# Kernel optimization log

Measured on AMD Instinct MI355X. Metric: run time of the kernel, lower is better.

The kernel has to match this reference:

```python
import jax, jax.numpy as jnp
import numpy as np

DIM = 2048
N_HEADS = 32
N_KV_HEADS = 8
HEAD_DIM = DIM // N_HEADS  # 64
N_REP = N_HEADS // N_KV_HEADS  # 4
SEQ = 2048
BSZ = 1


def _rope(x, cos, sin):
    # x: [b, s, h, hd]; cos/sin: [s, hd//2]
    x2 = x.reshape(*x.shape[:-1], HEAD_DIM // 2, 2)
    xe, xo = x2[..., 0], x2[..., 1]
    c = cos[None, :, None, :]
    s = sin[None, :, None, :]
    oe = xe * c - xo * s
    oo = xe * s + xo * c
    return jnp.stack([oe, oo], axis=-1).reshape(x.shape)


def setup_inputs() -> dict:
    key = jax.random.key(0)
    ks = jax.random.split(key, 6)
    x = jax.random.normal(ks[0], (BSZ, SEQ, DIM), dtype=jnp.float32)
    # llama-style rotary freqs
    inv = 1.0 / (10000.0 ** (np.arange(0, HEAD_DIM, 2, dtype=np.float32) / HEAD_DIM))
    t = np.arange(SEQ, dtype=np.float32)
    ang = np.outer(t, inv)  # [s, hd//2]
    freqs_cos = jnp.asarray(np.cos(ang))
    freqs_sin = jnp.asarray(np.sin(ang))
    # additive causal mask
    mask = jnp.where(jnp.tril(jnp.ones((SEQ, SEQ), bool)), 0.0, -jnp.inf).astype(jnp.float32)
    sc = 1.0 / np.sqrt(DIM)
    wq = jax.random.normal(ks[1], (DIM, N_HEADS * HEAD_DIM), jnp.float32) * sc
    wk = jax.random.normal(ks[2], (DIM, N_KV_HEADS * HEAD_DIM), jnp.float32) * sc
    wv = jax.random.normal(ks[3], (DIM, N_KV_HEADS * HEAD_DIM), jnp.float32) * sc
    wo = jax.random.normal(ks[4], (N_HEADS * HEAD_DIM, DIM), jnp.float32) * sc
    return {"x": x, "freqs_cos": freqs_cos, "freqs_sin": freqs_sin, "mask": mask,
            "wq": wq, "wk": wk, "wv": wv, "wo": wo}


def reference(x, freqs_cos, freqs_sin, mask, wq, wk, wv, wo):
    b, s, _ = x.shape
    xq = (x @ wq).reshape(b, s, N_HEADS, HEAD_DIM)
    xk = (x @ wk).reshape(b, s, N_KV_HEADS, HEAD_DIM)
    xv = (x @ wv).reshape(b, s, N_KV_HEADS, HEAD_DIM)
    xq = _rope(xq, freqs_cos, freqs_sin)
    xk = _rope(xk, freqs_cos, freqs_sin)
    # repeat_kv: expand kv heads by n_rep
    xk = jnp.repeat(xk, N_REP, axis=2)  # [b, s, H, hd]
    xv = jnp.repeat(xv, N_REP, axis=2)
    scores = jnp.einsum('bqhd,bkhd->bhqk', xq, xk) / np.sqrt(HEAD_DIM)
    scores = scores + mask[None, None, :, :]
    probs = jax.nn.softmax(scores.astype(jnp.float32), axis=-1).astype(xq.dtype)
    out = jnp.einsum('bhqk,bkhd->bqhd', probs, xv).reshape(b, s, N_HEADS * HEAD_DIM)
    return out @ wo
```

## Files before the change

kernel.cpp:

```cpp
#include <hip/hip_runtime.h>
#include <hip/hip_bf16.h>

#define SEQ  2048
#define DIM  2048
#define NQK  3072
#define NH   32
#define NKV  8
#define HD   64

typedef __attribute__((ext_vector_type(8))) short s8v;
typedef __attribute__((ext_vector_type(4))) short s4v;
typedef __attribute__((ext_vector_type(4))) float f32x4;

__device__ __forceinline__ short f2bf_bits(float f) {
    __hip_bfloat16 b = __float2bfloat16(f);
    short s; __builtin_memcpy(&s, &b, 2); return s;
}
__device__ __forceinline__ float bfbits2f(short s) {
    __hip_bfloat16 b; __builtin_memcpy(&b, &s, 2);
    return __bfloat162float(b);
}
__device__ __forceinline__ f32x4 mfma16(s8v a, s8v b, f32x4 c) {
    return __builtin_amdgcn_mfma_f32_16x16x32_bf16(a, b, c, 0, 0, 0);
}
__device__ __forceinline__ void load16_to_lds(const void* g, void* l) {
    __builtin_amdgcn_global_load_lds(
        (const __attribute__((address_space(1))) void*)g,
        (__attribute__((address_space(3))) void*)l, 16, 0, 0);
}

__global__ void cvt_f32_bf16(const float* __restrict__ src, short* __restrict__ dst) {
    int i = (blockIdx.x * 256 + threadIdx.x) * 4;
    float4 v = *(const float4*)(src + i);
    s4v o;
    o.x = f2bf_bits(v.x); o.y = f2bf_bits(v.y);
    o.z = f2bf_bits(v.z); o.w = f2bf_bits(v.w);
    *(s4v*)(dst + i) = o;
}

__global__ void transpose_cvt(const float* __restrict__ src, short* __restrict__ dst, int Cs) {
    __shared__ float tile[32][33];
    int bx = blockIdx.x * 32, by = blockIdx.y * 32;
    int tx = threadIdx.x, ty = threadIdx.y;
    #pragma unroll
    for (int j = 0; j < 32; j += 8)
        tile[ty + j][tx] = src[(size_t)(by + ty + j) * Cs + bx + tx];
    __syncthreads();
    #pragma unroll
    for (int j = 0; j < 32; j += 8)
        dst[(size_t)(bx + ty + j) * 2048 + by + tx] = f2bf_bits(tile[tx][ty + j]);
}

template<int MODE>
__global__ __launch_bounds__(256, 2)
void gemm_bt(const short* __restrict__ A, const short* __restrict__ BT,
             void* __restrict__ C, int M, int N, int K,
             short* __restrict__ vT,
             const float* __restrict__ fc, const float* __restrict__ fs)
{
    __shared__ short As[128 * 64];
    __shared__ short Bs[128 * 64];
    const int lane = threadIdx.x & 63;
    const int wid  = threadIdx.x >> 6;
    const int r = lane & 15, g = lane >> 4;
    const int bm = blockIdx.y * 128, bn = blockIdx.x * 128;
    const int wm = (wid >> 1) * 64, wn = (wid & 1) * 64;

    f32x4 acc[4][4];
    #pragma unroll
    for (int i = 0; i < 4; ++i)
        #pragma unroll
        for (int j = 0; j < 4; ++j) acc[i][j] = (f32x4){0.f, 0.f, 0.f, 0.f};

    const int srow = wid * 32 + (lane >> 3);
    const int scol = (lane & 7) * 8;

    for (int k0 = 0; k0 < K; k0 += 64) {
        #pragma unroll
        for (int s2 = 0; s2 < 4; ++s2) {
            int row = srow + s2 * 8;
            int seg = wid * 4 + s2;
            load16_to_lds(A  + (size_t)(bm + row) * K + k0 + scol, As + seg * 512);
            load16_to_lds(BT + (size_t)(bn + row) * K + k0 + scol, Bs + seg * 512);
        }
        __syncthreads();
        #pragma unroll
        for (int kk = 0; kk < 64; kk += 32) {
            s8v a[4], b[4];
            #pragma unroll
            for (int t = 0; t < 4; ++t)
                a[t] = *(const s8v*)&As[(wm + t * 16 + r) * 64 + kk + g * 8];
            #pragma unroll
            for (int t = 0; t < 4; ++t)
                b[t] = *(const s8v*)&Bs[(wn + t * 16 + r) * 64 + kk + g * 8];
            __builtin_amdgcn_s_setprio(1);
            #pragma unroll
            for (int i = 0; i < 4; ++i)
                #pragma unroll
                for (int j = 0; j < 4; ++j)
                    acc[i][j] = mfma16(a[i], b[j], acc[i][j]);
            __builtin_amdgcn_s_setprio(0);
        }
        __syncthreads();
    }

    if (MODE == 1) {
        #pragma unroll
        for (int i = 0; i < 4; ++i)
            #pragma unroll
            for (int j = 0; j < 4; ++j)
                #pragma unroll
                for (int q = 0; q < 4; ++q) {
                    int row = bm + wm + i * 16 + g * 4 + q;
                    int col = bn + wn + j * 16 + r;
                    ((float*)C)[(size_t)row * N + col] = acc[i][j][q];
                }
    } else {
        short* qkvO = (short*)C;
        if (bn >= 2560) {
            #pragma unroll
            for (int i = 0; i < 4; ++i)
                #pragma unroll
                for (int j = 0; j < 4; ++j) {
                    int row = bm + wm + i * 16 + g * 4;
                    int col = bn + wn + j * 16 + r - 2560;
                    s4v o;
                    #pragma unroll
                    for (int q = 0; q < 4; ++q) o[q] = f2bf_bits(acc[i][j][q]);
                    *(s4v*)&vT[(size_t)col * 2048 + row] = o;
                }
        } else {
            #pragma unroll
            for (int i = 0; i < 4; ++i)
                #pragma unroll
                for (int j = 0; j < 4; ++j) {
                    int row = bm + wm + i * 16 + g * 4;
                    int col = bn + wn + j * 16 + r;
                    int ii  = (col & 63) >> 1;
                    bool odd = (col & 1);
                    #pragma unroll
                    for (int q = 0; q < 4; ++q) {
                        float v = acc[i][j][q];
                        float p = __shfl_xor(v, 1, 64);
                        float c  = fc[(size_t)(row + q) * 32 + ii];
                        float sn = fs[(size_t)(row + q) * 32 + ii];
                        float outv = odd ? (p * sn + v * c) : (v * c - p * sn);
                        qkvO[(size_t)(row + q) * NQK + col] = f2bf_bits(outv);
                    }
                }
        }
    }
}

__global__ __launch_bounds__(256, 4)
void flash_attn(const short* __restrict__ qkv, const short* __restrict__ vT,
                short* __restrict__ O) {
    const int h  = blockIdx.x;
    const int qi = (int)gridDim.y - 1 - (int)blockIdx.y;
    const int qb = qi * 64;
    const int kh = h >> 2;
    const int lane = threadIdx.x & 63;
    const int wid  = threadIdx.x >> 6;
    const int r = lane & 15, g = lane >> 4;

    __shared__ short Ks[64][72];
    __shared__ short Vt[64][72];
    __shared__ short Pl[4][16][72];

    s8v qf0, qf1;
    {
        const short* qrow = qkv + (size_t)(qb + wid * 16 + r) * NQK + h * 64;
        qf0 = *(const s8v*)(qrow + g * 8);
        qf1 = *(const s8v*)(qrow + 32 + g * 8);
    }

    float m[4], l[4];
    f32x4 o[4];
    #pragma unroll
    for (int q = 0; q < 4; ++q) { m[q] = -1e30f; l[q] = 0.f; }
    #pragma unroll
    for (int t = 0; t < 4; ++t) o[t] = (f32x4){0.f, 0.f, 0.f, 0.f};

    const int tr = threadIdx.x >> 2;
    const int tc = (threadIdx.x & 3) * 16;

    const int nkt = qi + 1;
    for (int kt = 0; kt < nkt; ++kt) {
        {
            const short* kg = qkv + (size_t)(kt * 64 + tr) * NQK + 2048 + kh * 64 + tc;
            *(s8v*)&Ks[tr][tc]     = *(const s8v*)kg;
            *(s8v*)&Ks[tr][tc + 8] = *(const s8v*)(kg + 8);
            const short* vg = vT + (size_t)(kh * 64 + tr) * 2048 + kt * 64 + tc;
            *(s8v*)&Vt[tr][tc]     = *(const s8v*)vg;
            *(s8v*)&Vt[tr][tc + 8] = *(const s8v*)(vg + 8);
        }
        __syncthreads();

        f32x4 s[4];
        __builtin_amdgcn_s_setprio(1);
        #pragma unroll
        for (int t = 0; t < 4; ++t) {
            s8v kb0 = *(const s8v*)&Ks[t * 16 + r][g * 8];
            s8v kb1 = *(const s8v*)&Ks[t * 16 + r][32 + g * 8];
            f32x4 z = (f32x4){0.f, 0.f, 0.f, 0.f};
            z = mfma16(qf0, kb0, z);
            z = mfma16(qf1, kb1, z);
            s[t] = z;
        }
        __builtin_amdgcn_s_setprio(0);

        const bool diag = (kt == nkt - 1);
        #pragma unroll
        for (int t = 0; t < 4; ++t)
            #pragma unroll
            for (int q = 0; q < 4; ++q) {
                float v = s[t][q] * 0.125f;
                if (diag) {
                    int qrow = qb + wid * 16 + g * 4 + q;
                    int kpos = kt * 64 + t * 16 + r;
                    if (kpos > qrow) v = -1e30f;
                }
                s[t][q] = v;
            }

        float alpha[4];
        #pragma unroll
        for (int q = 0; q < 4; ++q) {
            float v = fmaxf(fmaxf(s[0][q], s[1][q]), fmaxf(s[2][q], s[3][q]));
            #pragma unroll
            for (int off = 1; off < 16; off <<= 1) v = fmaxf(v, __shfl_xor(v, off, 64));
            float mn = fmaxf(m[q], v);
            alpha[q] = __expf(m[q] - mn);
            m[q] = mn;
        }
        #pragma unroll
        for (int t = 0; t < 4; ++t)
            #pragma unroll
            for (int q = 0; q < 4; ++q)
                s[t][q] = __expf(s[t][q] - m[q]);
        #pragma unroll
        for (int q = 0; q < 4; ++q) {
            float v = s[0][q] + s[1][q] + s[2][q] + s[3][q];
            #pragma unroll
            for (int off = 1; off < 16; off <<= 1) v += __shfl_xor(v, off, 64);
            l[q] = l[q] * alpha[q] + v;
        }

        #pragma unroll
        for (int t = 0; t < 4; ++t)
            #pragma unroll
            for (int q = 0; q < 4; ++q) {
                o[t][q] *= alpha[q];
                Pl[wid][g * 4 + q][t * 16 + r] = f2bf_bits(s[t][q]);
            }
        asm volatile("s_waitcnt lgkmcnt(0)" ::: "memory");

        s8v pa0 = *(const s8v*)&Pl[wid][r][g * 8];
        s8v pa1 = *(const s8v*)&Pl[wid][r][32 + g * 8];
        __builtin_amdgcn_s_setprio(1);
        #pragma unroll
        for (int t = 0; t < 4; ++t) {
            s8v vb0 = *(const s8v*)&Vt[t * 16 + r][g * 8];
            s8v vb1 = *(const s8v*)&Vt[t * 16 + r][32 + g * 8];
            o[t] = mfma16(pa0, vb0, o[t]);
            o[t] = mfma16(pa1, vb1, o[t]);
        }
        __builtin_amdgcn_s_setprio(0);
        __syncthreads();
    }

    #pragma unroll
    for (int t = 0; t < 4; ++t)
        #pragma unroll
        for (int q = 0; q < 4; ++q) {
            float val = o[t][q] / l[q];
            O[(size_t)(qb + wid * 16 + g * 4 + q) * 2048 + h * 64 + t * 16 + r] = f2bf_bits(val);
        }
}

extern "C" void kernel_launch(void* const* d_in, const int* in_sizes, int n_in,
                              void* d_out, int out_size, void* d_ws, size_t ws_size,
                              hipStream_t stream)
{
    const float* x  = (const float*)d_in[0];
    const float* fc = (const float*)d_in[1];
    const float* fs = (const float*)d_in[2];
    const float* wq = (const float*)d_in[4];
    const float* wk = (const float*)d_in[5];
    const float* wv = (const float*)d_in[6];
    const float* wo = (const float*)d_in[7];
    float* out = (float*)d_out;

    char* ws = (char*)d_ws;
    short* xb    = (short*)(ws);
    short* wqkvT = (short*)(ws + 8  * 1024 * 1024);
    short* woT   = (short*)(ws + 20 * 1024 * 1024);
    short* qkv   = (short*)(ws + 28 * 1024 * 1024);
    short* vT    = (short*)(ws + 40 * 1024 * 1024);
    short* attnO = (short*)(ws + 42 * 1024 * 1024);

    dim3 tb(32, 8);
    cvt_f32_bf16<<<4096, 256, 0, stream>>>(x, xb);
    transpose_cvt<<<dim3(64, 64), tb, 0, stream>>>(wq, wqkvT, 2048);
    transpose_cvt<<<dim3(16, 64), tb, 0, stream>>>(wk, wqkvT + 2048 * 2048, 512);
    transpose_cvt<<<dim3(16, 64), tb, 0, stream>>>(wv, wqkvT + 2560 * 2048, 512);
    transpose_cvt<<<dim3(64, 64), tb, 0, stream>>>(wo, woT, 2048);

    gemm_bt<0><<<dim3(24, 16), 256, 0, stream>>>(xb, wqkvT, qkv, 2048, 3072, 2048, vT, fc, fs);
    flash_attn<<<dim3(32, 32), 256, 0, stream>>>(qkv, vT, attnO);
    gemm_bt<1><<<dim3(16, 16), 256, 0, stream>>>(attnO, woT, out, 2048, 2048, 2048, nullptr, nullptr, nullptr);
}
```

Measured before the change: 287.8 us.

## Retile GEMMs to 128x64 with XCD swizzle and widen flash-attn to 128 query rows

The GEMM tile shrinks to 128x64 and the grid becomes 1D, with a swizzle that groups consecutive workgroups per XCD. The launch-bounds occupancy target rises to 3, giving more blocks for better CU fill. Flash attention now handles 128 query rows per block, each wave doing two 16-row slices, so every K/V tile loaded into LDS is reused by twice as many queries. The softmax moves to exp2 with the log2e factor folded into the scale, and skips the rescale unless the running max grows by more than 8. Larger attention blocks halve the grid, which can worsen load imbalance on the causal triangle, and the extra accumulators raise register pressure.

```diff
diff --git a/kernel.cpp b/kernel.cpp
--- a/kernel.cpp
+++ b/kernel.cpp
@@ -27,6 +27,9 @@
     __builtin_amdgcn_global_load_lds(
         (const __attribute__((address_space(1))) void*)g,
         (__attribute__((address_space(3))) void*)l, 16, 0, 0);
+}
+__device__ __forceinline__ float fexp2(float x) {
+    float y; asm("v_exp_f32 %0, %1" : "=v"(y) : "v"(x)); return y;
 }
 
 __global__ void cvt_f32_bf16(const float* __restrict__ src, short* __restrict__ dst) {
@@ -52,52 +55,60 @@
 }
 
 template<int MODE>
-__global__ __launch_bounds__(256, 2)
+__global__ __launch_bounds__(256, 3)
 void gemm_bt(const short* __restrict__ A, const short* __restrict__ BT,
-             void* __restrict__ C, int M, int N, int K,
+             void* __restrict__ C, int M, int N, int K, int nx,
              short* __restrict__ vT,
              const float* __restrict__ fc, const float* __restrict__ fs)
 {
     __shared__ short As[128 * 64];
-    __shared__ short Bs[128 * 64];
+    __shared__ short Bs[64 * 64];
+    const int nwg = gridDim.x;
+    const int orig = blockIdx.x;
+    const int wg = (orig & 7) * (nwg >> 3) + (orig >> 3);
+    const int bx = wg % nx, by = wg / nx;
+    const int bm = by * 128, bn = bx * 64;
+
     const int lane = threadIdx.x & 63;
     const int wid  = threadIdx.x >> 6;
     const int r = lane & 15, g = lane >> 4;
-    const int bm = blockIdx.y * 128, bn = blockIdx.x * 128;
-    const int wm = (wid >> 1) * 64, wn = (wid & 1) * 64;
-
-    f32x4 acc[4][4];
+    const int wm = (wid >> 1) * 64, wn = (wid & 1) * 32;
+
+    f32x4 acc[4][2];
     #pragma unroll
     for (int i = 0; i < 4; ++i)
         #pragma unroll
-        for (int j = 0; j < 4; ++j) acc[i][j] = (f32x4){0.f, 0.f, 0.f, 0.f};
-
-    const int srow = wid * 32 + (lane >> 3);
+        for (int j = 0; j < 2; ++j) acc[i][j] = (f32x4){0.f, 0.f, 0.f, 0.f};
+
+    const int srl = lane >> 3;
     const int scol = (lane & 7) * 8;
 
     for (int k0 = 0; k0 < K; k0 += 64) {
         #pragma unroll
         for (int s2 = 0; s2 < 4; ++s2) {
-            int row = srow + s2 * 8;
-            int seg = wid * 4 + s2;
-            load16_to_lds(A  + (size_t)(bm + row) * K + k0 + scol, As + seg * 512);
-            load16_to_lds(BT + (size_t)(bn + row) * K + k0 + scol, Bs + seg * 512);
+            int row = wid * 32 + s2 * 8 + srl;
+            load16_to_lds(A + (size_t)(bm + row) * K + k0 + scol, As + (wid * 4 + s2) * 512);
+        }
+        #pragma unroll
+        for (int s2 = 0; s2 < 2; ++s2) {
+            int row = wid * 16 + s2 * 8 + srl;
+            load16_to_lds(BT + (size_t)(bn + row) * K + k0 + scol, Bs + (wid * 2 + s2) * 512);
         }
         __syncthreads();
         #pragma unroll
         for (int kk = 0; kk < 64; kk += 32) {
-            s8v a[4], b[4];
+            s8v a[4], b[2];
             #pragma unroll
             for (int t = 0; t < 4; ++t)
                 a[t] = *(const s8v*)&As[(wm + t * 16 + r) * 64 + kk + g * 8];
             #pragma unroll
-            for (int t = 0; t < 4; ++t)
+            for (int t = 0; t < 2; ++t)
                 b[t] = *(const s8v*)&Bs[(wn + t * 16 + r) * 64 + kk + g * 8];
             __builtin_amdgcn_s_setprio(1);
             #pragma unroll
             for (int i = 0; i < 4; ++i)
                 #pragma unroll
-                for (int j = 0; j < 4; ++j)
+                for (int j = 0; j < 2; ++j)
                     acc[i][j] = mfma16(a[i], b[j], acc[i][j]);
             __builtin_amdgcn_s_setprio(0);
         }
@@ -108,7 +119,7 @@
         #pragma unroll
         for (int i = 0; i < 4; ++i)
             #pragma unroll
-            for (int j = 0; j < 4; ++j)
+            for (int j = 0; j < 2; ++j)
                 #pragma unroll
                 for (int q = 0; q < 4; ++q) {
                     int row = bm + wm + i * 16 + g * 4 + q;
@@ -121,7 +132,7 @@
             #pragma unroll
             for (int i = 0; i < 4; ++i)
                 #pragma unroll
-                for (int j = 0; j < 4; ++j) {
+                for (int j = 0; j < 2; ++j) {
                     int row = bm + wm + i * 16 + g * 4;
                     int col = bn + wn + j * 16 + r - 2560;
                     s4v o;
@@ -133,7 +144,7 @@
             #pragma unroll
             for (int i = 0; i < 4; ++i)
                 #pragma unroll
-                for (int j = 0; j < 4; ++j) {
+                for (int j = 0; j < 2; ++j) {
                     int row = bm + wm + i * 16 + g * 4;
                     int col = bn + wn + j * 16 + r;
                     int ii  = (col & 63) >> 1;
@@ -152,12 +163,13 @@
     }
 }
 
+#define SCL 0.18033688f
 __global__ __launch_bounds__(256, 4)
 void flash_attn(const short* __restrict__ qkv, const short* __restrict__ vT,
                 short* __restrict__ O) {
     const int h  = blockIdx.x;
     const int qi = (int)gridDim.y - 1 - (int)blockIdx.y;
-    const int qb = qi * 64;
+    const int qb = qi * 128;
     const int kh = h >> 2;
     const int lane = threadIdx.x & 63;
     const int wid  = threadIdx.x >> 6;
@@ -165,26 +177,31 @@
 
     __shared__ short Ks[64][72];
     __shared__ short Vt[64][72];
-    __shared__ short Pl[4][16][72];
-
-    s8v qf0, qf1;
-    {
-        const short* qrow = qkv + (size_t)(qb + wid * 16 + r) * NQK + h * 64;
-        qf0 = *(const s8v*)(qrow + g * 8);
-        qf1 = *(const s8v*)(qrow + 32 + g * 8);
-    }
-
-    float m[4], l[4];
-    f32x4 o[4];
-    #pragma unroll
-    for (int q = 0; q < 4; ++q) { m[q] = -1e30f; l[q] = 0.f; }
-    #pragma unroll
-    for (int t = 0; t < 4; ++t) o[t] = (f32x4){0.f, 0.f, 0.f, 0.f};
+    __shared__ short Pl[4][32][72];
+
+    s8v qf[2][2];
+    #pragma unroll
+    for (int i = 0; i < 2; ++i) {
+        const short* qrow = qkv + (size_t)(qb + wid * 32 + i * 16 + r) * NQK + h * 64;
+        qf[i][0] = *(const s8v*)(qrow + g * 8);
+        qf[i][1] = *(const s8v*)(qrow + 32 + g * 8);
+    }
+
+    float m[2][4], l[2][4];
+    f32x4 o[2][4];
+    #pragma unroll
+    for (int i = 0; i < 2; ++i)
+        #pragma unroll
+        for (int q = 0; q < 4; ++q) { m[i][q] = -1e30f; l[i][q] = 0.f; }
+    #pragma unroll
+    for (int i = 0; i < 2; ++i)
+        #pragma unroll
+        for (int t = 0; t < 4; ++t) o[i][t] = (f32x4){0.f, 0.f, 0.f, 0.f};
 
     const int tr = threadIdx.x >> 2;
     const int tc = (threadIdx.x & 3) * 16;
 
-    const int nkt = qi + 1;
+    const int nkt = 2 * qi + 2;
     for (int kt = 0; kt < nkt; ++kt) {
         {
             const short* kg = qkv + (size_t)(kt * 64 + tr) * NQK + 2048 + kh * 64 + tc;
@@ -196,86 +213,106 @@
         }
         __syncthreads();
 
-        f32x4 s[4];
+        const bool diag = (kt >= nkt - 2);
+        #pragma unroll
+        for (int i = 0; i < 2; ++i) {
+            f32x4 s[4];
+            __builtin_amdgcn_s_setprio(1);
+            #pragma unroll
+            for (int t = 0; t < 4; ++t) {
+                s8v kb0 = *(const s8v*)&Ks[t * 16 + r][g * 8];
+                s8v kb1 = *(const s8v*)&Ks[t * 16 + r][32 + g * 8];
+                f32x4 z = (f32x4){0.f, 0.f, 0.f, 0.f};
+                z = mfma16(qf[i][0], kb0, z);
+                z = mfma16(qf[i][1], kb1, z);
+                s[t] = z;
+            }
+            __builtin_amdgcn_s_setprio(0);
+
+            #pragma unroll
+            for (int t = 0; t < 4; ++t)
+                #pragma unroll
+                for (int q = 0; q < 4; ++q) {
+                    float v = s[t][q] * SCL;
+                    if (diag) {
+                        int qrow = qb + wid * 32 + i * 16 + g * 4 + q;
+                        int kpos = kt * 64 + t * 16 + r;
+                        if (kpos > qrow) v = -1e30f;
+                    }
+                    s[t][q] = v;
+                }
+
+            float pm[4];
+            #pragma unroll
+            for (int q = 0; q < 4; ++q) {
+                float v = fmaxf(fmaxf(s[0][q], s[1][q]), fmaxf(s[2][q], s[3][q]));
+                #pragma unroll
+                for (int off = 1; off < 16; off <<= 1) v = fmaxf(v, __shfl_xor(v, off, 64));
+                pm[q] = v;
+            }
+            bool need = (pm[0] > m[i][0] + 8.f) || (pm[1] > m[i][1] + 8.f) ||
+                        (pm[2] > m[i][2] + 8.f) || (pm[3] > m[i][3] + 8.f);
+            if (__any(need)) {
+                #pragma unroll
+                for (int q = 0; q < 4; ++q) {
+                    float mn = fmaxf(m[i][q], pm[q]);
+                    float al = fexp2(m[i][q] - mn);
+                    m[i][q] = mn;
+                    l[i][q] *= al;
+                    #pragma unroll
+                    for (int t = 0; t < 4; ++t) o[i][t][q] *= al;
+                }
+            }
+            #pragma unroll
+            for (int t = 0; t < 4; ++t)
+                #pragma unroll
+                for (int q = 0; q < 4; ++q)
+                    s[t][q] = fexp2(s[t][q] - m[i][q]);
+            #pragma unroll
+            for (int q = 0; q < 4; ++q) {
+                float v = (s[0][q] + s[1][q]) + (s[2][q] + s[3][q]);
+                #pragma unroll
+                for (int off = 1; off < 16; off <<= 1) v += __shfl_xor(v, off, 64);
+                l[i][q] += v;
+            }
+            #pragma unroll
+            for (int t = 0; t < 4; ++t)
+                #pragma unroll
+                for (int q = 0; q < 4; ++q)
+                    Pl[wid][i * 16 + g * 4 + q][t * 16 + r] = f2bf_bits(s[t][q]);
+        }
+        asm volatile("s_waitcnt lgkmcnt(0)" ::: "memory");
+
         __builtin_amdgcn_s_setprio(1);
         #pragma unroll
-        for (int t = 0; t < 4; ++t) {
-            s8v kb0 = *(const s8v*)&Ks[t * 16 + r][g * 8];
-            s8v kb1 = *(const s8v*)&Ks[t * 16 + r][32 + g * 8];
-            f32x4 z = (f32x4){0.f, 0.f, 0.f, 0.f};
-            z = mfma16(qf0, kb0, z);
-            z = mfma16(qf1, kb1, z);
-            s[t] = z;
-        }
-        __builtin_amdgcn_s_setprio(0);
-
-        const bool diag = (kt == nkt - 1);
-        #pragma unroll
-        for (int t = 0; t < 4; ++t)
-            #pragma unroll
-            for (int q = 0; q < 4; ++q) {
-                float v = s[t][q] * 0.125f;
-                if (diag) {
-                    int qrow = qb + wid * 16 + g * 4 + q;
-                    int kpos = kt * 64 + t * 16 + r;
-                    if (kpos > qrow) v = -1e30f;
-                }
-                s[t][q] = v;
-            }
-
-        float alpha[4];
-        #pragma unroll
-        for (int q = 0; q < 4; ++q) {
-            float v = fmaxf(fmaxf(s[0][q], s[1][q]), fmaxf(s[2][q], s[3][q]));
-            #pragma unroll
-            for (int off = 1; off < 16; off <<= 1) v = fmaxf(v, __shfl_xor(v, off, 64));
-            float mn = fmaxf(m[q], v);
-            alpha[q] = __expf(m[q] - mn);
-            m[q] = mn;
-        }
-        #pragma unroll
-        for (int t = 0; t < 4; ++t)
-            #pragma unroll
-            for (int q = 0; q < 4; ++q)
-                s[t][q] = __expf(s[t][q] - m[q]);
-        #pragma unroll
-        for (int q = 0; q < 4; ++q) {
-            float v = s[0][q] + s[1][q] + s[2][q] + s[3][q];
-            #pragma unroll
-            for (int off = 1; off < 16; off <<= 1) v += __shfl_xor(v, off, 64);
-            l[q] = l[q] * alpha[q] + v;
-        }
-
-        #pragma unroll
-        for (int t = 0; t < 4; ++t)
-            #pragma unroll
-            for (int q = 0; q < 4; ++q) {
-                o[t][q] *= alpha[q];
-                Pl[wid][g * 4 + q][t * 16 + r] = f2bf_bits(s[t][q]);
-            }
-        asm volatile("s_waitcnt lgkmcnt(0)" ::: "memory");
-
-        s8v pa0 = *(const s8v*)&Pl[wid][r][g * 8];
-        s8v pa1 = *(const s8v*)&Pl[wid][r][32 + g * 8];
-        __builtin_amdgcn_s_setprio(1);
-        #pragma unroll
-        for (int t = 0; t < 4; ++t) {
-            s8v vb0 = *(const s8v*)&Vt[t * 16 + r][g * 8];
-            s8v vb1 = *(const s8v*)&Vt[t * 16 + r][32 + g * 8];
-            o[t] = mfma16(pa0, vb0, o[t]);
-            o[t] = mfma16(pa1, vb1, o[t]);
+        for (int i = 0; i < 2; ++i) {
+            s8v pa0 = *(const s8v*)&Pl[wid][i * 16 + r][g * 8];
+            s8v pa1 = *(const s8v*)&Pl[wid][i * 16 + r][32 + g * 8];
+            #pragma unroll
+            for (int t = 0; t < 4; ++t) {
+                s8v vb0 = *(const s8v*)&Vt[t * 16 + r][g * 8];
+                s8v vb1 = *(const s8v*)&Vt[t * 16 + r][32 + g * 8];
+                o[i][t] = mfma16(pa0, vb0, o[i][t]);
+                o[i][t] = mfma16(pa1, vb1, o[i][t]);
+            }
         }
         __builtin_amdgcn_s_setprio(0);
         __syncthreads();
     }
 
     #pragma unroll
-    for (int t = 0; t < 4; ++t)
-        #pragma unroll
-        for (int q = 0; q < 4; ++q) {
-            float val = o[t][q] / l[q];
-            O[(size_t)(qb + wid * 16 + g * 4 + q) * 2048 + h * 64 + t * 16 + r] = f2bf_bits(val);
-        }
+    for (int i = 0; i < 2; ++i) {
+        float rl[4];
+        #pragma unroll
+        for (int q = 0; q < 4; ++q) rl[q] = __builtin_amdgcn_rcpf(l[i][q]);
+        #pragma unroll
+        for (int t = 0; t < 4; ++t)
+            #pragma unroll
+            for (int q = 0; q < 4; ++q) {
+                float val = o[i][t][q] * rl[q];
+                O[(size_t)(qb + wid * 32 + i * 16 + g * 4 + q) * 2048 + h * 64 + t * 16 + r] = f2bf_bits(val);
+            }
+    }
 }
 
 extern "C" void kernel_launch(void* const* d_in, const int* in_sizes, int n_in,
@@ -306,7 +343,7 @@
     transpose_cvt<<<dim3(16, 64), tb, 0, stream>>>(wv, wqkvT + 2560 * 2048, 512);
     transpose_cvt<<<dim3(64, 64), tb, 0, stream>>>(wo, woT, 2048);
 
-    gemm_bt<0><<<dim3(24, 16), 256, 0, stream>>>(xb, wqkvT, qkv, 2048, 3072, 2048, vT, fc, fs);
-    flash_attn<<<dim3(32, 32), 256, 0, stream>>>(qkv, vT, attnO);
-    gemm_bt<1><<<dim3(16, 16), 256, 0, stream>>>(attnO, woT, out, 2048, 2048, 2048, nullptr, nullptr, nullptr);
-}
+    gemm_bt<0><<<768, 256, 0, stream>>>(xb, wqkvT, qkv, 2048, 3072, 2048, 48, vT, fc, fs);
+    flash_attn<<<dim3(32, 16), 256, 0, stream>>>(qkv, vT, attnO);
+    gemm_bt<1><<<512, 256, 0, stream>>>(attnO, woT, out, 2048, 2048, 2048, 32, nullptr, nullptr, nullptr);
+}
```

Result: slower. 300.8 us (+4.5%).

## Split-K GEMMs with XCD-aware remap, separate RoPE/add kernels, lazy softmax rescale

Applied to the files above, without the earlier changes.

Both projection GEMMs now use split-K by two, writing bf16 partials to two buffers. The workgroup index is remapped across XCDs, and occupancy is raised to 3 per CU. New kernels sum the partials and apply RoPE, the V transpose and the final fp32 output, which adds memory traffic and extra launches. Flash attention moves to exp2 with a folded log2e scale, skips rescaling unless the running max grows by more than 8, and replaces the division with a reciprocal. Summing partials in bf16 adds rounding error.

```diff
diff --git a/kernel.cpp b/kernel.cpp
--- a/kernel.cpp
+++ b/kernel.cpp
@@ -27,6 +27,9 @@
     __builtin_amdgcn_global_load_lds(
         (const __attribute__((address_space(1))) void*)g,
         (__attribute__((address_space(3))) void*)l, 16, 0, 0);
+}
+__device__ __forceinline__ float fexp2(float x) {
+    float y; asm("v_exp_f32 %0, %1" : "=v"(y) : "v"(x)); return y;
 }
 
 __global__ void cvt_f32_bf16(const float* __restrict__ src, short* __restrict__ dst) {
@@ -51,19 +54,23 @@
         dst[(size_t)(bx + ty + j) * 2048 + by + tx] = f2bf_bits(tile[tx][ty + j]);
 }
 
-template<int MODE>
-__global__ __launch_bounds__(256, 2)
+__global__ __launch_bounds__(256, 3)
 void gemm_bt(const short* __restrict__ A, const short* __restrict__ BT,
-             void* __restrict__ C, int M, int N, int K,
-             short* __restrict__ vT,
-             const float* __restrict__ fc, const float* __restrict__ fs)
+             short* __restrict__ P0, short* __restrict__ P1,
+             int N, int K, int nx)
 {
     __shared__ short As[128 * 64];
     __shared__ short Bs[128 * 64];
+    const int nwg = gridDim.x;
+    const int orig = blockIdx.x;
+    const int wg = (orig & 7) * (nwg >> 3) + (orig >> 3);
+    const int ks  = wg & 1;
+    const int bxy = wg >> 1;
+    const int bm = (bxy / nx) * 128, bn = (bxy % nx) * 128;
+
     const int lane = threadIdx.x & 63;
     const int wid  = threadIdx.x >> 6;
     const int r = lane & 15, g = lane >> 4;
-    const int bm = blockIdx.y * 128, bn = blockIdx.x * 128;
     const int wm = (wid >> 1) * 64, wn = (wid & 1) * 64;
 
     f32x4 acc[4][4];
@@ -74,8 +81,9 @@
 
     const int srow = wid * 32 + (lane >> 3);
     const int scol = (lane & 7) * 8;
-
-    for (int k0 = 0; k0 < K; k0 += 64) {
+    const int kbeg = ks * (K >> 1), kend = kbeg + (K >> 1);
+
+    for (int k0 = kbeg; k0 < kend; k0 += 64) {
         #pragma unroll
         for (int s2 = 0; s2 < 4; ++s2) {
             int row = srow + s2 * 8;
@@ -104,54 +112,77 @@
         __syncthreads();
     }
 
-    if (MODE == 1) {
-        #pragma unroll
-        for (int i = 0; i < 4; ++i)
-            #pragma unroll
-            for (int j = 0; j < 4; ++j)
-                #pragma unroll
-                for (int q = 0; q < 4; ++q) {
-                    int row = bm + wm + i * 16 + g * 4 + q;
-                    int col = bn + wn + j * 16 + r;
-                    ((float*)C)[(size_t)row * N + col] = acc[i][j][q];
-                }
-    } else {
-        short* qkvO = (short*)C;
-        if (bn >= 2560) {
-            #pragma unroll
-            for (int i = 0; i < 4; ++i)
-                #pragma unroll
-                for (int j = 0; j < 4; ++j) {
-                    int row = bm + wm + i * 16 + g * 4;
-                    int col = bn + wn + j * 16 + r - 2560;
-                    s4v o;
-                    #pragma unroll
-                    for (int q = 0; q < 4; ++q) o[q] = f2bf_bits(acc[i][j][q]);
-                    *(s4v*)&vT[(size_t)col * 2048 + row] = o;
-                }
-        } else {
-            #pragma unroll
-            for (int i = 0; i < 4; ++i)
-                #pragma unroll
-                for (int j = 0; j < 4; ++j) {
-                    int row = bm + wm + i * 16 + g * 4;
-                    int col = bn + wn + j * 16 + r;
-                    int ii  = (col & 63) >> 1;
-                    bool odd = (col & 1);
-                    #pragma unroll
-                    for (int q = 0; q < 4; ++q) {
-                        float v = acc[i][j][q];
-                        float p = __shfl_xor(v, 1, 64);
-                        float c  = fc[(size_t)(row + q) * 32 + ii];
-                        float sn = fs[(size_t)(row + q) * 32 + ii];
-                        float outv = odd ? (p * sn + v * c) : (v * c - p * sn);
-                        qkvO[(size_t)(row + q) * NQK + col] = f2bf_bits(outv);
-                    }
-                }
-        }
-    }
-}
-
+    short* P = ks ? P1 : P0;
+    #pragma unroll
+    for (int i = 0; i < 4; ++i)
+        #pragma unroll
+        for (int j = 0; j < 4; ++j)
+            #pragma unroll
+            for (int q = 0; q < 4; ++q) {
+                int row = bm + wm + i * 16 + g * 4 + q;
+                int col = bn + wn + j * 16 + r;
+                P[(size_t)row * N + col] = f2bf_bits(acc[i][j][q]);
+            }
+}
+
+__global__ void rope_add(const short* __restrict__ P0, const short* __restrict__ P1,
+                         short* __restrict__ qkv,
+                         const float* __restrict__ fc, const float* __restrict__ fs) {
+    int idx = blockIdx.x * 256 + threadIdx.x;
+    int row = idx / 320;
+    int col = (idx - row * 320) * 8;
+    s8v a = *(const s8v*)(P0 + (size_t)row * NQK + col);
+    s8v b = *(const s8v*)(P1 + (size_t)row * NQK + col);
+    int p0 = (col & 63) >> 1;
+    s8v o;
+    #pragma unroll
+    for (int k = 0; k < 4; ++k) {
+        float xe = bfbits2f(a[2 * k])     + bfbits2f(b[2 * k]);
+        float xo = bfbits2f(a[2 * k + 1]) + bfbits2f(b[2 * k + 1]);
+        float c  = fc[row * 32 + p0 + k];
+        float sn = fs[row * 32 + p0 + k];
+        o[2 * k]     = f2bf_bits(xe * c - xo * sn);
+        o[2 * k + 1] = f2bf_bits(xe * sn + xo * c);
+    }
+    *(s8v*)(qkv + (size_t)row * NQK + col) = o;
+}
+
+__global__ void vT_add(const short* __restrict__ P0, const short* __restrict__ P1,
+                       short* __restrict__ vT) {
+    __shared__ float tile[32][33];
+    int bx = blockIdx.x * 32;
+    int by = blockIdx.y * 32;
+    int tx = threadIdx.x, ty = threadIdx.y;
+    #pragma unroll
+    for (int j = 0; j < 32; j += 8) {
+        size_t off = (size_t)(by + ty + j) * NQK + 2560 + bx + tx;
+        tile[ty + j][tx] = bfbits2f(P0[off]) + bfbits2f(P1[off]);
+    }
+    __syncthreads();
+    #pragma unroll
+    for (int j = 0; j < 32; j += 8)
+        vT[(size_t)(bx + ty + j) * 2048 + by + tx] = f2bf_bits(tile[tx][ty + j]);
+}
+
+__global__ void add_out(const short* __restrict__ R0, const short* __restrict__ R1,
+                        float* __restrict__ out) {
+    int i = (blockIdx.x * 256 + threadIdx.x) * 8;
+    s8v a = *(const s8v*)(R0 + i);
+    s8v b = *(const s8v*)(R1 + i);
+    float4 o0, o1;
+    o0.x = bfbits2f(a[0]) + bfbits2f(b[0]);
+    o0.y = bfbits2f(a[1]) + bfbits2f(b[1]);
+    o0.z = bfbits2f(a[2]) + bfbits2f(b[2]);
+    o0.w = bfbits2f(a[3]) + bfbits2f(b[3]);
+    o1.x = bfbits2f(a[4]) + bfbits2f(b[4]);
+    o1.y = bfbits2f(a[5]) + bfbits2f(b[5]);
+    o1.z = bfbits2f(a[6]) + bfbits2f(b[6]);
+    o1.w = bfbits2f(a[7]) + bfbits2f(b[7]);
+    *(float4*)(out + i)     = o0;
+    *(float4*)(out + i + 4) = o1;
+}
+
+#define SCL 0.18033688f
 __global__ __launch_bounds__(256, 4)
 void flash_attn(const short* __restrict__ qkv, const short* __restrict__ vT,
                 short* __restrict__ O) {
@@ -214,7 +245,7 @@
         for (int t = 0; t < 4; ++t)
             #pragma unroll
             for (int q = 0; q < 4; ++q) {
-                float v = s[t][q] * 0.125f;
+                float v = s[t][q] * SCL;
                 if (diag) {
                     int qrow = qb + wid * 16 + g * 4 + q;
                     int kpos = kt * 64 + t * 16 + r;
@@ -223,36 +254,44 @@
                 s[t][q] = v;
             }
 
-        float alpha[4];
+        float pm[4];
         #pragma unroll
         for (int q = 0; q < 4; ++q) {
             float v = fmaxf(fmaxf(s[0][q], s[1][q]), fmaxf(s[2][q], s[3][q]));
             #pragma unroll
             for (int off = 1; off < 16; off <<= 1) v = fmaxf(v, __shfl_xor(v, off, 64));
-            float mn = fmaxf(m[q], v);
-            alpha[q] = __expf(m[q] - mn);
-            m[q] = mn;
+            pm[q] = v;
+        }
+        bool need = (pm[0] > m[0] + 8.f) || (pm[1] > m[1] + 8.f) ||
+                    (pm[2] > m[2] + 8.f) || (pm[3] > m[3] + 8.f);
+        if (__any(need)) {
+            #pragma unroll
+            for (int q = 0; q < 4; ++q) {
+                float mn = fmaxf(m[q], pm[q]);
+                float al = fexp2(m[q] - mn);
+                m[q] = mn;
+                l[q] *= al;
+                #pragma unroll
+                for (int t = 0; t < 4; ++t) o[t][q] *= al;
+            }
         }
         #pragma unroll
         for (int t = 0; t < 4; ++t)
             #pragma unroll
             for (int q = 0; q < 4; ++q)
-                s[t][q] = __expf(s[t][q] - m[q]);
+                s[t][q] = fexp2(s[t][q] - m[q]);
         #pragma unroll
         for (int q = 0; q < 4; ++q) {
-            float v = s[0][q] + s[1][q] + s[2][q] + s[3][q];
+            float v = (s[0][q] + s[1][q]) + (s[2][q] + s[3][q]);
             #pragma unroll
             for (int off = 1; off < 16; off <<= 1) v += __shfl_xor(v, off, 64);
-            l[q] = l[q] * alpha[q] + v;
-        }
-
+            l[q] += v;
+        }
         #pragma unroll
         for (int t = 0; t < 4; ++t)
             #pragma unroll
-            for (int q = 0; q < 4; ++q) {
-                o[t][q] *= alpha[q];
+            for (int q = 0; q < 4; ++q)
                 Pl[wid][g * 4 + q][t * 16 + r] = f2bf_bits(s[t][q]);
-            }
         asm volatile("s_waitcnt lgkmcnt(0)" ::: "memory");
 
         s8v pa0 = *(const s8v*)&Pl[wid][r][g * 8];
@@ -269,11 +308,14 @@
         __syncthreads();
     }
 
+    float rl[4];
+    #pragma unroll
+    for (int q = 0; q < 4; ++q) rl[q] = __builtin_amdgcn_rcpf(l[q]);
     #pragma unroll
     for (int t = 0; t < 4; ++t)
         #pragma unroll
         for (int q = 0; q < 4; ++q) {
-            float val = o[t][q] / l[q];
+            float val = o[t][q] * rl[q];
             O[(size_t)(qb + wid * 16 + g * 4 + q) * 2048 + h * 64 + t * 16 + r] = f2bf_bits(val);
         }
 }
@@ -298,6 +340,8 @@
     short* qkv   = (short*)(ws + 28 * 1024 * 1024);
     short* vT    = (short*)(ws + 40 * 1024 * 1024);
     short* attnO = (short*)(ws + 42 * 1024 * 1024);
+    short* P0    = (short*)(ws + 50 * 1024 * 1024);
+    short* P1    = (short*)(ws + 63 * 1024 * 1024);
 
     dim3 tb(32, 8);
     cvt_f32_bf16<<<4096, 256, 0, stream>>>(x, xb);
@@ -306,7 +350,12 @@
     transpose_cvt<<<dim3(16, 64), tb, 0, stream>>>(wv, wqkvT + 2560 * 2048, 512);
     transpose_cvt<<<dim3(64, 64), tb, 0, stream>>>(wo, woT, 2048);
 
-    gemm_bt<0><<<dim3(24, 16), 256, 0, stream>>>(xb, wqkvT, qkv, 2048, 3072, 2048, vT, fc, fs);
+    gemm_bt<<<768, 256, 0, stream>>>(xb, wqkvT, P0, P1, 3072, 2048, 24);
+    rope_add<<<2560, 256, 0, stream>>>(P0, P1, qkv, fc, fs);
+    vT_add<<<dim3(16, 64), tb, 0, stream>>>(P0, P1, vT);
+
     flash_attn<<<dim3(32, 32), 256, 0, stream>>>(qkv, vT, attnO);
-    gemm_bt<1><<<dim3(16, 16), 256, 0, stream>>>(attnO, woT, out, 2048, 2048, 2048, nullptr, nullptr, nullptr);
-}
+
+    gemm_bt<<<512, 256, 0, stream>>>(attnO, woT, P0, P1, 2048, 2048, 16);
+    add_out<<<2048, 256, 0, stream>>>(P0, P1, out);
+}
```

After: 272.3 us. 1.06x faster.
